# Performance work log

Measured on AMD Instinct MI355X. Metric: run time of the kernel, lower is better.

## Reference

```python
import jax, jax.numpy as jnp
import numpy as np

K = 3          # kernel_size
EPS = 1e-12    # epsilon from l2_normal and abs-clamp


def setup_inputs() -> dict:
    key = jax.random.key(0)
    k1, k2 = jax.random.split(key)
    B, H, W, C, F = 8, 224, 224, 32, 32
    image = jax.random.normal(k1, (B, H, W, C), dtype=jnp.float32)
    # glorot-uniform-ish weight, shape (1, C*K*K, filters)
    fan = C * K * K + F
    lim = np.sqrt(6.0 / fan).astype(np.float32)
    w = jax.random.uniform(k2, (1, C * K * K, F), dtype=jnp.float32, minval=-lim, maxval=lim)
    p = jnp.full((F,), 100.0 ** 0.5, dtype=jnp.float32)   # p init = sqrt(100)
    q = jnp.full((1,), 10.0 ** 0.5, dtype=jnp.float32)    # q init = sqrt(10)
    return {"image": image, "w": w, "p": p, "q": q}


def reference(image, w, p, q):
    # CosSim2D, kernel_size=3, stride=1, padding='same', non-depthwise.
    B, H, W, C = image.shape
    pad = K // 2
    padded = jnp.pad(image, ((0, 0), (pad, pad), (pad, pad), (0, 0)))
    # im2col: kernel-position-major, channel-minor -> matches tf.stack(axis=3) + reshape
    patches = jnp.stack(
        [padded[:, dy:dy + H, dx:dx + W, :] for dy in range(K) for dx in range(K)],
        axis=3,
    )  # (B, H, W, K*K, C)
    x = patches.reshape(B, H * W, K * K * C)
    q_term = jnp.square(q) / 10.0                       # scalar (broadcast)
    x_norm = jnp.sqrt(jnp.maximum(jnp.sum(x * x, axis=2, keepdims=True), EPS)) + q_term
    w_norm = jnp.sqrt(jnp.maximum(jnp.sum(w * w, axis=1, keepdims=True), EPS)) + q_term
    sim = jnp.matmul(x / x_norm, (w / w_norm)[0])       # (B, H*W, filters)
    out = jnp.sign(sim) * jnp.power(jnp.abs(sim) + EPS, jnp.square(p) / 100.0)
    return out.reshape(B, H, W, -1)
```

## Files before the change

kernel.cpp:

```cpp
#include <hip/hip_runtime.h>
#include <hip/hip_bf16.h>


#define H_ 224
#define W_ 224
#define C_ 32
#define F_ 32

#define NSTEP 18
#define HROWS 10
#define HCOLS 34

typedef __bf16 bf16_t;
typedef bf16_t bf16x8 __attribute__((ext_vector_type(8)));
typedef float f32x16 __attribute__((ext_vector_type(16)));

#define WFRAG_BYTES (NSTEP * 64 * 8 * 2)

__global__ __launch_bounds__(256) void cos2d_prep(
    const float* __restrict__ w, const float* __restrict__ p,
    const float* __restrict__ q, bf16_t* __restrict__ wfrag,
    float* __restrict__ winv, float* __restrict__ ef) {
  __shared__ float part[8][32];
  const int tid = threadIdx.x;
  const int f = tid & 31, kg = tid >> 5;
  float s = 0.f;
#pragma unroll
  for (int i = 0; i < 36; ++i) {
    const float v = w[(kg + 8 * i) * F_ + f];
    s += v * v;
  }
  part[kg][f] = s;
  __syncthreads();
  if (tid < 32) {
    float t = 0.f;
#pragma unroll
    for (int g = 0; g < 8; ++g) t += part[g][tid];
    const float qt = q[0] * q[0] * 0.1f;
    winv[tid] = 1.f / (sqrtf(fmaxf(t, 1e-12f)) + qt);
    ef[tid] = p[tid] * p[tid] * 0.01f;
  }
  for (int t = tid; t < NSTEP * 64; t += 256) {
    const int s2 = t >> 6, l = t & 63;
    const int ff = l & 31;
    union { bf16_t v[8]; uint4 u; } tv;
#pragma unroll
    for (int e = 0; e < 8; ++e) {
      const int kk = s2 * 16 + ((l >> 5) << 3) + e;
      tv.v[e] = (bf16_t)w[kk * F_ + ff];
    }
    *(uint4*)(wfrag + (size_t)t * 8) = tv.u;
  }
}

__global__ __launch_bounds__(256, 4) void cos2d_main(
    const float* __restrict__ img, const bf16_t* __restrict__ wfrag,
    const float* __restrict__ winv, const float* __restrict__ ef,
    const float* __restrict__ q, float* __restrict__ out) {
  __shared__ bf16_t xt[HROWS][HCOLS][40];
  __shared__ float ssum[HROWS][HCOLS];

  const int tid = threadIdx.x;
  const int lane = tid & 63;
  const int wv = tid >> 6;
  const int lp = lane & 31;

  const int bid = blockIdx.x;
  const int tw = bid % 7;
  const int th = (bid / 7) % 28;
  const int b  = bid / 196;
  const int h0 = th * 8, w0 = tw * 32;

  const float qt = q[0] * q[0] * 0.1f;
  const float efv = ef[lp];
  const float wnv = winv[lp];

  bf16x8 bfrag[NSTEP];
  const bf16x8* wf4 = (const bf16x8*)wfrag;
#pragma unroll
  for (int s2 = 0; s2 < NSTEP; ++s2) bfrag[s2] = wf4[s2 * 64 + lane];

  for (int idx = tid; idx < HROWS * HCOLS * 8; idx += 256) {
    const int p = idx >> 3, sub = idx & 7;
    const int rr = p / HCOLS, cc = p - rr * HCOLS;
    const int hh = h0 - 1 + rr, wc = w0 - 1 + cc;
    float4 v = make_float4(0.f, 0.f, 0.f, 0.f);
    if ((unsigned)hh < H_ && (unsigned)wc < W_)
      v = *(const float4*)(img + ((size_t)(b * H_ + hh) * W_ + wc) * C_ + sub * 4);
    float s = v.x * v.x + v.y * v.y + v.z * v.z + v.w * v.w;
    s += __shfl_xor(s, 1);
    s += __shfl_xor(s, 2);
    s += __shfl_xor(s, 4);
    union { bf16_t h[4]; uint2 u; } pk;
    pk.h[0] = (bf16_t)v.x; pk.h[1] = (bf16_t)v.y;
    pk.h[2] = (bf16_t)v.z; pk.h[3] = (bf16_t)v.w;
    *(uint2*)&xt[rr][cc][sub * 4] = pk.u;
    if (sub == 0) ssum[rr][cc] = s;
  }
  __syncthreads();

  const int mr0 = wv * 2;

  float xinv[2];
#pragma unroll
  for (int t = 0; t < 2; ++t) {
    const int mr = mr0 + t;
    const float xn2 = ssum[mr + 0][lp] + ssum[mr + 0][lp + 1] + ssum[mr + 0][lp + 2]
                    + ssum[mr + 1][lp] + ssum[mr + 1][lp + 1] + ssum[mr + 1][lp + 2]
                    + ssum[mr + 2][lp] + ssum[mr + 2][lp + 1] + ssum[mr + 2][lp + 2];
    xinv[t] = 1.f / (sqrtf(fmaxf(xn2, 1e-12f)) + qt);
  }

  f32x16 acc0, acc1;
#pragma unroll
  for (int i = 0; i < 16; ++i) { acc0[i] = 0.f; acc1[i] = 0.f; }

#pragma unroll
  for (int s2 = 0; s2 < NSTEP; ++s2) {
    const int pos = s2 >> 1;
    const int dy = pos / 3, dx = pos - dy * 3;
    const int chof = (s2 & 1) * 16 + ((lane >> 5) << 3);
    const bf16x8 a0 = *(const bf16x8*)&xt[mr0 + 0 + dy][lp + dx][chof];
    const bf16x8 a1 = *(const bf16x8*)&xt[mr0 + 1 + dy][lp + dx][chof];
    acc0 = __builtin_amdgcn_mfma_f32_32x32x16_bf16(a0, bfrag[s2], acc0, 0, 0, 0);
    acc1 = __builtin_amdgcn_mfma_f32_32x32x16_bf16(a1, bfrag[s2], acc1, 0, 0, 0);
  }

#pragma unroll
  for (int t = 0; t < 2; ++t) {
    const f32x16& acc = t ? acc1 : acc0;
    const int obase = (b * H_ + h0 + mr0 + t) * W_ + w0;
#pragma unroll
    for (int jj = 0; jj < 16; ++jj) {
      const int row = (jj & 3) + 8 * (jj >> 2) + 4 * (lane >> 5);
      const float xi = __shfl(xinv[t], row);
      const float sim = acc[jj] * xi * wnv;
      const float ps = fabsf(sim) + 1e-12f;
      float r = exp2f(efv * __log2f(ps));
      r = copysignf(r, sim);
      out[(size_t)(obase + row) * F_ + lp] = r;
    }
  }
}

extern "C" void kernel_launch(void* const* d_in, const int* in_sizes, int n_in,
                              void* d_out, int out_size, void* d_ws, size_t ws_size,
                              hipStream_t stream) {
  const float* img = (const float*)d_in[0];
  const float* w   = (const float*)d_in[1];
  const float* p   = (const float*)d_in[2];
  const float* q   = (const float*)d_in[3];

  bf16_t* wfrag = (bf16_t*)d_ws;
  float*  winv  = (float*)((char*)d_ws + WFRAG_BYTES);
  float*  ef    = winv + 64;

  cos2d_prep<<<1, 256, 0, stream>>>(w, p, q, wfrag, winv, ef);
  cos2d_main<<<1568, 256, 0, stream>>>(img, wfrag, winv, ef, q, (float*)d_out);
}
```

Measured before the change: 37.77 us.

## Add exponent-one fast path, nontemporal stores, split prep kernel, raise occupancy

Adds a runtime check that every per-filter exponent equals one and, when it does, skips the log2/exp2 power computation in the epilogue. Output writes become nontemporal stores. The weight-prep kernel now runs across several blocks instead of one. Weight fragments are loaded per MFMA step instead of preloaded into registers, and the launch bound is raised to five blocks per SM. The fast path follows the p initialisation in the test inputs but is guarded, so it stays correct for other values; fetching weight fragments inside the loop may add load latency in exchange for lower register pressure.

```diff
diff --git a/kernel.cpp b/kernel.cpp
--- a/kernel.cpp
+++ b/kernel.cpp
@@ -10,6 +10,7 @@
 #define NSTEP 18
 #define HROWS 10
 #define HCOLS 34
+#define SLOTS (HROWS * HCOLS * 8)
 
 typedef __bf16 bf16_t;
 typedef bf16_t bf16x8 __attribute__((ext_vector_type(8)));
@@ -21,39 +22,43 @@
     const float* __restrict__ w, const float* __restrict__ p,
     const float* __restrict__ q, bf16_t* __restrict__ wfrag,
     float* __restrict__ winv, float* __restrict__ ef) {
-  __shared__ float part[8][32];
   const int tid = threadIdx.x;
-  const int f = tid & 31, kg = tid >> 5;
-  float s = 0.f;
+  if (blockIdx.x == 0) {
+    __shared__ float part[8][32];
+    const int f = tid & 31, kg = tid >> 5;
+    float s = 0.f;
 #pragma unroll
-  for (int i = 0; i < 36; ++i) {
-    const float v = w[(kg + 8 * i) * F_ + f];
-    s += v * v;
-  }
-  part[kg][f] = s;
-  __syncthreads();
-  if (tid < 32) {
-    float t = 0.f;
+    for (int i = 0; i < 36; ++i) {
+      const float v = w[(kg + 8 * i) * F_ + f];
+      s += v * v;
+    }
+    part[kg][f] = s;
+    __syncthreads();
+    if (tid < 32) {
+      float t = 0.f;
 #pragma unroll
-    for (int g = 0; g < 8; ++g) t += part[g][tid];
-    const float qt = q[0] * q[0] * 0.1f;
-    winv[tid] = 1.f / (sqrtf(fmaxf(t, 1e-12f)) + qt);
-    ef[tid] = p[tid] * p[tid] * 0.01f;
-  }
-  for (int t = tid; t < NSTEP * 64; t += 256) {
-    const int s2 = t >> 6, l = t & 63;
-    const int ff = l & 31;
-    union { bf16_t v[8]; uint4 u; } tv;
+      for (int g = 0; g < 8; ++g) t += part[g][tid];
+      const float qt = q[0] * q[0] * 0.1f;
+      winv[tid] = 1.f / (sqrtf(fmaxf(t, 1e-12f)) + qt);
+      ef[tid] = p[tid] * p[tid] * 0.01f;
+    }
+  } else {
+    const int t = (blockIdx.x - 1) * 256 + tid;
+    if (t < NSTEP * 64) {
+      const int s2 = t >> 6, l = t & 63;
+      const int ff = l & 31;
+      union { bf16_t v[8]; uint4 u; } tv;
 #pragma unroll
-    for (int e = 0; e < 8; ++e) {
-      const int kk = s2 * 16 + ((l >> 5) << 3) + e;
-      tv.v[e] = (bf16_t)w[kk * F_ + ff];
+      for (int e = 0; e < 8; ++e) {
+        const int kk = s2 * 16 + ((l >> 5) << 3) + e;
+        tv.v[e] = (bf16_t)w[kk * F_ + ff];
+      }
+      *(uint4*)(wfrag + (size_t)t * 8) = tv.u;
     }
-    *(uint4*)(wfrag + (size_t)t * 8) = tv.u;
   }
 }
 
-__global__ __launch_bounds__(256, 4) void cos2d_main(
+__global__ __launch_bounds__(256, 5) void cos2d_main(
     const float* __restrict__ img, const bf16_t* __restrict__ wfrag,
     const float* __restrict__ winv, const float* __restrict__ ef,
     const float* __restrict__ q, float* __restrict__ out) {
@@ -74,15 +79,11 @@
   const float qt = q[0] * q[0] * 0.1f;
   const float efv = ef[lp];
   const float wnv = winv[lp];
+  const bool allfast = __all(__builtin_fabsf(efv - 1.0f) < 1e-6f);
 
-  bf16x8 bfrag[NSTEP];
-  const bf16x8* wf4 = (const bf16x8*)wfrag;
-#pragma unroll
-  for (int s2 = 0; s2 < NSTEP; ++s2) bfrag[s2] = wf4[s2 * 64 + lane];
-
-  for (int idx = tid; idx < HROWS * HCOLS * 8; idx += 256) {
-    const int p = idx >> 3, sub = idx & 7;
-    const int rr = p / HCOLS, cc = p - rr * HCOLS;
+  for (int idx = tid; idx < SLOTS; idx += 256) {
+    const int pp = idx >> 3, sub = idx & 7;
+    const int rr = pp / HCOLS, cc = pp - rr * HCOLS;
     const int hh = h0 - 1 + rr, wc = w0 - 1 + cc;
     float4 v = make_float4(0.f, 0.f, 0.f, 0.f);
     if ((unsigned)hh < H_ && (unsigned)wc < W_)
@@ -105,9 +106,10 @@
 #pragma unroll
   for (int t = 0; t < 2; ++t) {
     const int mr = mr0 + t;
-    const float xn2 = ssum[mr + 0][lp] + ssum[mr + 0][lp + 1] + ssum[mr + 0][lp + 2]
-                    + ssum[mr + 1][lp] + ssum[mr + 1][lp + 1] + ssum[mr + 1][lp + 2]
-                    + ssum[mr + 2][lp] + ssum[mr + 2][lp + 1] + ssum[mr + 2][lp + 2];
+    const float xn2 =
+        ssum[mr + 0][lp] + ssum[mr + 0][lp + 1] + ssum[mr + 0][lp + 2] +
+        ssum[mr + 1][lp] + ssum[mr + 1][lp + 1] + ssum[mr + 1][lp + 2] +
+        ssum[mr + 2][lp] + ssum[mr + 2][lp + 1] + ssum[mr + 2][lp + 2];
     xinv[t] = 1.f / (sqrtf(fmaxf(xn2, 1e-12f)) + qt);
   }
 
@@ -115,30 +117,43 @@
 #pragma unroll
   for (int i = 0; i < 16; ++i) { acc0[i] = 0.f; acc1[i] = 0.f; }
 
+  const bf16x8* wf4 = (const bf16x8*)wfrag;
 #pragma unroll
   for (int s2 = 0; s2 < NSTEP; ++s2) {
+    const bf16x8 bf = wf4[s2 * 64 + lane];
     const int pos = s2 >> 1;
     const int dy = pos / 3, dx = pos - dy * 3;
     const int chof = (s2 & 1) * 16 + ((lane >> 5) << 3);
     const bf16x8 a0 = *(const bf16x8*)&xt[mr0 + 0 + dy][lp + dx][chof];
     const bf16x8 a1 = *(const bf16x8*)&xt[mr0 + 1 + dy][lp + dx][chof];
-    acc0 = __builtin_amdgcn_mfma_f32_32x32x16_bf16(a0, bfrag[s2], acc0, 0, 0, 0);
-    acc1 = __builtin_amdgcn_mfma_f32_32x32x16_bf16(a1, bfrag[s2], acc1, 0, 0, 0);
+    acc0 = __builtin_amdgcn_mfma_f32_32x32x16_bf16(a0, bf, acc0, 0, 0, 0);
+    acc1 = __builtin_amdgcn_mfma_f32_32x32x16_bf16(a1, bf, acc1, 0, 0, 0);
   }
 
 #pragma unroll
   for (int t = 0; t < 2; ++t) {
     const f32x16& acc = t ? acc1 : acc0;
     const int obase = (b * H_ + h0 + mr0 + t) * W_ + w0;
+    if (allfast) {
 #pragma unroll
-    for (int jj = 0; jj < 16; ++jj) {
-      const int row = (jj & 3) + 8 * (jj >> 2) + 4 * (lane >> 5);
-      const float xi = __shfl(xinv[t], row);
-      const float sim = acc[jj] * xi * wnv;
-      const float ps = fabsf(sim) + 1e-12f;
-      float r = exp2f(efv * __log2f(ps));
-      r = copysignf(r, sim);
-      out[(size_t)(obase + row) * F_ + lp] = r;
+      for (int jj = 0; jj < 16; ++jj) {
+        const int row = (jj & 3) + 8 * (jj >> 2) + 4 * (lane >> 5);
+        const float xi = __shfl(xinv[t], row);
+        const float sim = acc[jj] * xi * wnv;
+        const float r = copysignf(fabsf(sim) + 1e-12f, sim);
+        __builtin_nontemporal_store(r, &out[(size_t)(obase + row) * F_ + lp]);
+      }
+    } else {
+#pragma unroll
+      for (int jj = 0; jj < 16; ++jj) {
+        const int row = (jj & 3) + 8 * (jj >> 2) + 4 * (lane >> 5);
+        const float xi = __shfl(xinv[t], row);
+        const float sim = acc[jj] * xi * wnv;
+        const float ps = fabsf(sim) + 1e-12f;
+        float r = exp2f(efv * __log2f(ps));
+        r = copysignf(r, sim);
+        __builtin_nontemporal_store(r, &out[(size_t)(obase + row) * F_ + lp]);
+      }
     }
   }
 }
@@ -155,6 +170,6 @@
   float*  winv  = (float*)((char*)d_ws + WFRAG_BYTES);
   float*  ef    = winv + 64;
 
-  cos2d_prep<<<1, 256, 0, stream>>>(w, p, q, wfrag, winv, ef);
+  cos2d_prep<<<6, 256, 0, stream>>>(w, p, q, wfrag, winv, ef);
   cos2d_main<<<1568, 256, 0, stream>>>(img, wfrag, winv, ef, q, (float*)d_out);
 }
```

New measurement: 34.54 us. 1.09x faster.
